# Kernel tuning notes

Hardware: AMD Instinct MI355X
Metric: run time of the kernel (lower is better)

The kernel has to match this reference:

```python
import jax, jax.numpy as jnp
import numpy as np

B, N, DIM, H = 8, 2048, 64, 8  # per-head dim == DIM (module convention: inner_dim = dim * n_heads)


def setup_inputs() -> dict:
    key = jax.random.key(0)
    k1, k2, k3 = jax.random.split(key, 3)
    x = jax.random.normal(k1, (B, N, DIM), dtype=jnp.float32)
    W_qkv = jax.random.normal(k2, (DIM, 3 * H * DIM), dtype=jnp.float32) * (DIM ** -0.5)
    W_out = jax.random.normal(k3, (H * DIM, DIM), dtype=jnp.float32) * ((H * DIM) ** -0.5)
    b_out = jnp.zeros((DIM,), dtype=jnp.float32)
    return {"x": x, "W_qkv": W_qkv, "W_out": W_out, "b_out": b_out}


def reference(x, W_qkv, W_out, b_out):
    b, n, d = x.shape
    h = W_qkv.shape[1] // (3 * d)
    qkv = x @ W_qkv                                   # [b, n, 3*h*d]
    q, k, v = jnp.split(qkv, 3, axis=-1)              # each [b, n, h*d]
    def to_heads(t):
        return t.reshape(b, n, h, d).transpose(0, 2, 1, 3)  # [b, h, n, d]
    q, k, v = map(to_heads, (q, k, v))
    scale = d ** -0.5
    dot = jnp.einsum('bhid,bhjd->bhij', q, k) * scale  # [b, h, n, n]
    A = jax.nn.softmax(dot, axis=-1)
    z = jnp.einsum('bhij,bhjd->bhid', A, v)            # [b, h, n, d]
    z = z.transpose(0, 2, 1, 3).reshape(b, n, h * d)   # [b, n, h*d]
    return z @ W_out + b_out                           # [b, n, d]
```

## Files before the change

### kernel.cpp

```cpp
#include <hip/hip_runtime.h>
#include <math.h>

#define BB 8
#define NN 2048
#define DD 64
#define HH 8
#define BH (BB*HH)
#define HD (HH*DD)
#define NROWS (BB*NN)
#define QKV_COLS (3*HD)

typedef __bf16 bf16_8 __attribute__((ext_vector_type(8)));
typedef __bf16 bf16_4 __attribute__((ext_vector_type(4)));
typedef float  f32_16 __attribute__((ext_vector_type(16)));
typedef float  f32_4  __attribute__((ext_vector_type(4)));

__device__ __forceinline__ unsigned pack_bf16(float a, float b) {
  union { __bf16 h[2]; unsigned u; } t;
  t.h[0] = (__bf16)a; t.h[1] = (__bf16)b;
  return t.u;
}

__global__ __launch_bounds__(256) void wtrans_kernel(
    const float* __restrict__ Wqkv, const float* __restrict__ Wout,
    __bf16* __restrict__ Wtq, __bf16* __restrict__ Wto) {
  int idx = blockIdx.x * 256 + threadIdx.x;
  if (idx < 64 * QKV_COLS) {
    int k = idx / QKV_COLS, col = idx % QKV_COLS;
    float v = Wqkv[idx];
    if (col < HD) v *= 0.125f;
    Wtq[col * 64 + k] = (__bf16)v;
  } else {
    int j = idx - 64 * QKV_COLS;
    int k = j >> 6, col = j & 63;
    Wto[col * 512 + k] = (__bf16)Wout[j];
  }
}

__global__ __launch_bounds__(256) void qkv_kernel(
    const float* __restrict__ x, const __bf16* __restrict__ Wtq,
    __bf16* __restrict__ Q, __bf16* __restrict__ K, __bf16* __restrict__ V) {
  const int lane = threadIdx.x & 63;
  const int wave = threadIdx.x >> 6;
  const int l31  = lane & 31, lhi = lane >> 5;
  const int cg   = blockIdx.x;
  const int row0 = blockIdx.y * 128 + wave * 32;

  const float* xr = x + (size_t)(row0 + l31) * 64 + lhi * 8;
  bf16_8 af[4];
#pragma unroll
  for (int s = 0; s < 4; s++) {
    f32_4 a0 = *(const f32_4*)(xr + s * 16);
    f32_4 a1 = *(const f32_4*)(xr + s * 16 + 4);
#pragma unroll
    for (int j = 0; j < 4; j++) { af[s][j] = (__bf16)a0[j]; af[s][4 + j] = (__bf16)a1[j]; }
  }

  f32_16 C0, C1;
#pragma unroll
  for (int i = 0; i < 16; i++) { C0[i] = 0.f; C1[i] = 0.f; }

  const __bf16* wb = Wtq + (size_t)cg * 64 * 64 + lhi * 8;
#pragma unroll
  for (int s = 0; s < 4; s++) {
    bf16_8 b0 = *(const bf16_8*)(wb + (size_t)l31 * 64 + s * 16);
    bf16_8 b1 = *(const bf16_8*)(wb + (size_t)(32 + l31) * 64 + s * 16);
    C0 = __builtin_amdgcn_mfma_f32_32x32x16_bf16(af[s], b0, C0, 0, 0, 0);
    C1 = __builtin_amdgcn_mfma_f32_32x32x16_bf16(af[s], b1, C1, 0, 0, 0);
  }

  const int col0  = cg * 64;
  const int which = col0 >> 9;
  const int h     = (col0 >> 6) & 7;
  __bf16* dst = (which == 0) ? Q : ((which == 1) ? K : V);
#pragma unroll
  for (int r = 0; r < 16; r++) {
    int n  = row0 + (r & 3) + 8 * (r >> 2) + 4 * lhi;
    int b  = n >> 11;
    int nn = n & 2047;
    size_t base = (((size_t)(b * HH + h) * NN) + nn) * DD;
    dst[base + l31]      = (__bf16)C0[r];
    dst[base + 32 + l31] = (__bf16)C1[r];
  }
}

__global__ __launch_bounds__(256) void vtrans_kernel(
    const __bf16* __restrict__ V, __bf16* __restrict__ Vt) {
  __shared__ __bf16 T[64 * 72];
  const int bh = blockIdx.x >> 5;
  const int n0 = (blockIdx.x & 31) * 64;
  const __bf16* src = V  + (size_t)bh * NN * DD;
  __bf16*       dst = Vt + (size_t)bh * DD * NN;

#pragma unroll
  for (int i = 0; i < 2; i++) {
    int c = threadIdx.x + i * 256;
    int r = c >> 3, c8 = (c & 7) * 8;
    *(bf16_8*)(&T[r * 72 + c8]) = *(const bf16_8*)(src + (size_t)(n0 + r) * DD + c8);
  }
  __syncthreads();
#pragma unroll
  for (int i = 0; i < 2; i++) {
    int c = threadIdx.x + i * 256;
    int d = c >> 3, j8 = (c & 7) * 8;
    bf16_8 o;
#pragma unroll
    for (int j = 0; j < 8; j++) o[j] = T[(j8 + j) * 72 + d];
    *(bf16_8*)(dst + (size_t)d * NN + n0 + j8) = o;
  }
}

__global__ __launch_bounds__(256, 4) void attn_kernel(
    const __bf16* __restrict__ Q, const __bf16* __restrict__ K,
    const __bf16* __restrict__ Vt, __bf16* __restrict__ z) {
  __shared__ __bf16 Ks[64 * 72];
  __shared__ __bf16 Vs[64 * 72];

  const int tid  = threadIdx.x;
  const int wave = tid >> 6;
  const int lane = tid & 63;
  const int l31  = lane & 31;
  const int lhi  = lane >> 5;
  const int xl   = lane ^ 32;
  const int bh   = blockIdx.x >> 4;
  const int q0   = (blockIdx.x & 15) * 128 + wave * 32;

  const __bf16* Qbase = Q + ((size_t)bh * NN + q0 + l31) * DD + lhi * 8;
  bf16_8 qf[4];
#pragma unroll
  for (int s = 0; s < 4; s++) qf[s] = *(const bf16_8*)(Qbase + s * 16);

  f32_16 O0, O1;
#pragma unroll
  for (int i = 0; i < 16; i++) { O0[i] = 0.f; O1[i] = 0.f; }
  float lsum = 0.f;

  const __bf16* Kb = K  + (size_t)bh * NN * DD;
  const __bf16* Vb = Vt + (size_t)bh * DD * NN;

  for (int kt = 0; kt < NN; kt += 64) {
    __syncthreads();
#pragma unroll
    for (int i = 0; i < 2; i++) {
      int c = tid + i * 256;
      int r = c >> 3, c8 = (c & 7) * 8;
      *(bf16_8*)(&Ks[r * 72 + c8]) = *(const bf16_8*)(Kb + (size_t)(kt + r) * DD + c8);
      *(bf16_8*)(&Vs[r * 72 + c8]) = *(const bf16_8*)(Vb + (size_t)r * NN + kt + c8);
    }
    __syncthreads();

    f32_16 S0, S1;
#pragma unroll
    for (int i = 0; i < 16; i++) { S0[i] = 0.f; S1[i] = 0.f; }
#pragma unroll
    for (int s = 0; s < 4; s++) {
      bf16_8 kb0 = *(const bf16_8*)(&Ks[l31 * 72 + s * 16 + lhi * 8]);
      bf16_8 kb1 = *(const bf16_8*)(&Ks[(32 + l31) * 72 + s * 16 + lhi * 8]);
      S0 = __builtin_amdgcn_mfma_f32_32x32x16_bf16(kb0, qf[s], S0, 0, 0, 0);
      S1 = __builtin_amdgcn_mfma_f32_32x32x16_bf16(kb1, qf[s], S1, 0, 0, 0);
    }

    unsigned pk[16];
#pragma unroll
    for (int t = 0; t < 8; t++) {
      float a = __expf(S0[2 * t]), b = __expf(S0[2 * t + 1]);
      float c = __expf(S1[2 * t]), d = __expf(S1[2 * t + 1]);
      lsum += (a + b) + (c + d);
      pk[t]     = pack_bf16(a, b);
      pk[8 + t] = pack_bf16(c, d);
    }

#pragma unroll
    for (int half = 0; half < 2; half++) {
#pragma unroll
      for (int st = 0; st < 2; st++) {
        const int base = half * 8 + st * 4;
        unsigned a0 = pk[base + 0], a1 = pk[base + 1];
        unsigned a2 = pk[base + 2], a3 = pk[base + 3];
        unsigned w0 = (unsigned)__shfl((int)a0, xl, 64);
        unsigned w1 = (unsigned)__shfl((int)a1, xl, 64);
        unsigned w2 = (unsigned)__shfl((int)a2, xl, 64);
        unsigned w3 = (unsigned)__shfl((int)a3, xl, 64);
        union { unsigned u[4]; bf16_8 v; } F;
        F.u[0] = lhi ? w2 : a0;
        F.u[1] = lhi ? w3 : a1;
        F.u[2] = lhi ? a2 : w0;
        F.u[3] = lhi ? a3 : w1;
        const int ks = half * 2 + st;
        bf16_8 va0 = *(const bf16_8*)(&Vs[l31 * 72 + ks * 16 + lhi * 8]);
        bf16_8 va1 = *(const bf16_8*)(&Vs[(32 + l31) * 72 + ks * 16 + lhi * 8]);
        O0 = __builtin_amdgcn_mfma_f32_32x32x16_bf16(va0, F.v, O0, 0, 0, 0);
        O1 = __builtin_amdgcn_mfma_f32_32x32x16_bf16(va1, F.v, O1, 0, 0, 0);
      }
    }
  }

  lsum += __shfl_xor(lsum, 32, 64);
  const float inv = 1.f / lsum;

  __syncthreads();
  __bf16* ow = ((wave & 2) ? Vs : Ks) + (wave & 1) * (32 * 72);
#pragma unroll
  for (int g = 0; g < 4; g++) {
    bf16_4 p0, p1;
#pragma unroll
    for (int i = 0; i < 4; i++) {
      p0[i] = (__bf16)(O0[4 * g + i] * inv);
      p1[i] = (__bf16)(O1[4 * g + i] * inv);
    }
    const int d0 = 8 * g + 4 * lhi;
    *(bf16_4*)(ow + l31 * 72 + d0)      = p0;
    *(bf16_4*)(ow + l31 * 72 + 32 + d0) = p1;
  }
  __syncthreads();

  const int b = bh >> 3, h = bh & 7;
  const int qr = lane >> 1, c0 = (lane & 1) * 32;
  __bf16* zp = z + ((size_t)b * NN + q0 + qr) * HD + h * DD + c0;
#pragma unroll
  for (int j = 0; j < 4; j++) {
    *(bf16_8*)(zp + 8 * j) = *(const bf16_8*)(ow + qr * 72 + c0 + 8 * j);
  }
}

__global__ __launch_bounds__(64) void out_proj_kernel(
    const __bf16* __restrict__ z, const __bf16* __restrict__ Wto,
    const float* __restrict__ bout, float* __restrict__ out) {
  const int lane = threadIdx.x;
  const int l31  = lane & 31, lhi = lane >> 5;
  const int row0 = blockIdx.x * 32;

  const __bf16* zr = z   + (size_t)(row0 + l31) * HD + lhi * 8;
  const __bf16* w0 = Wto + (size_t)l31 * HD + lhi * 8;
  const __bf16* w1 = Wto + (size_t)(32 + l31) * HD + lhi * 8;

  f32_16 C0, C1;
#pragma unroll
  for (int i = 0; i < 16; i++) { C0[i] = 0.f; C1[i] = 0.f; }

#pragma unroll
  for (int s = 0; s < 32; s++) {
    bf16_8 a  = *(const bf16_8*)(zr + s * 16);
    bf16_8 b0 = *(const bf16_8*)(w0 + s * 16);
    bf16_8 b1 = *(const bf16_8*)(w1 + s * 16);
    C0 = __builtin_amdgcn_mfma_f32_32x32x16_bf16(a, b0, C0, 0, 0, 0);
    C1 = __builtin_amdgcn_mfma_f32_32x32x16_bf16(a, b1, C1, 0, 0, 0);
  }

  const float bi0 = bout[l31];
  const float bi1 = bout[32 + l31];
#pragma unroll
  for (int r = 0; r < 16; r++) {
    int n = row0 + (r & 3) + 8 * (r >> 2) + 4 * lhi;
    out[(size_t)n * 64 + l31]      = C0[r] + bi0;
    out[(size_t)n * 64 + 32 + l31] = C1[r] + bi1;
  }
}

extern "C" void kernel_launch(void* const* d_in, const int* in_sizes, int n_in,
                              void* d_out, int out_size, void* d_ws, size_t ws_size,
                              hipStream_t stream) {
  const float* x    = (const float*)d_in[0];
  const float* Wqkv = (const float*)d_in[1];
  const float* Wout = (const float*)d_in[2];
  const float* bout = (const float*)d_in[3];
  float* out = (float*)d_out;

  const size_t buf_elems = (size_t)BB * HH * NN * DD;
  __bf16* Qw  = (__bf16*)d_ws;
  __bf16* Kw  = Qw  + buf_elems;
  __bf16* Vw  = Kw  + buf_elems;
  __bf16* Vtw = Vw  + buf_elems;
  __bf16* zw  = Vtw + buf_elems;
  __bf16* Wtq = zw  + buf_elems;
  __bf16* Wto = Wtq + (size_t)QKV_COLS * 64;

  wtrans_kernel<<<512, 256, 0, stream>>>(Wqkv, Wout, Wtq, Wto);
  qkv_kernel<<<dim3(QKV_COLS / 64, NROWS / 128), 256, 0, stream>>>(x, Wtq, Qw, Kw, Vw);
  vtrans_kernel<<<BH * (NN / 64), 256, 0, stream>>>(Vw, Vtw);
  attn_kernel<<<BH * (NN / 128), 256, 0, stream>>>(Qw, Kw, Vtw, zw);
  out_proj_kernel<<<NROWS / 32, 64, 0, stream>>>(zw, Wto, bout, out);
}
```

Baseline: 206.5 us.

## Fuse V transpose into QKV, prefetch 128-key tiles, use exp2 and permlane swap

```diff
diff --git a/kernel.cpp b/kernel.cpp
--- a/kernel.cpp
+++ b/kernel.cpp
@@ -14,11 +14,20 @@
 typedef __bf16 bf16_4 __attribute__((ext_vector_type(4)));
 typedef float  f32_16 __attribute__((ext_vector_type(16)));
 typedef float  f32_4  __attribute__((ext_vector_type(4)));
+typedef int    i32_2  __attribute__((ext_vector_type(2)));
 
 __device__ __forceinline__ unsigned pack_bf16(float a, float b) {
   union { __bf16 h[2]; unsigned u; } t;
   t.h[0] = (__bf16)a; t.h[1] = (__bf16)b;
   return t.u;
+}
+
+__device__ __forceinline__ float fast_exp2(float x) {
+#if __has_builtin(__builtin_amdgcn_exp2f)
+  return __builtin_amdgcn_exp2f(x);
+#else
+  return __expf(x * 0.69314718056f);
+#endif
 }
 
 __global__ __launch_bounds__(256) void wtrans_kernel(
@@ -28,8 +37,9 @@
   if (idx < 64 * QKV_COLS) {
     int k = idx / QKV_COLS, col = idx % QKV_COLS;
     float v = Wqkv[idx];
-    if (col < HD) v *= 0.125f;
+    if (col < HD) v *= 0.125f * 1.44269504088896f;
     Wtq[col * 64 + k] = (__bf16)v;
+    (void)k;
   } else {
     int j = idx - 64 * QKV_COLS;
     int k = j >> 6, col = j & 63;
@@ -39,7 +49,8 @@
 
 __global__ __launch_bounds__(256) void qkv_kernel(
     const float* __restrict__ x, const __bf16* __restrict__ Wtq,
-    __bf16* __restrict__ Q, __bf16* __restrict__ K, __bf16* __restrict__ V) {
+    __bf16* __restrict__ Q, __bf16* __restrict__ K, __bf16* __restrict__ Vt) {
+  __shared__ __bf16 T[4][64][34];
   const int lane = threadIdx.x & 63;
   const int wave = threadIdx.x >> 6;
   const int l31  = lane & 31, lhi = lane >> 5;
@@ -72,49 +83,39 @@
   const int col0  = cg * 64;
   const int which = col0 >> 9;
   const int h     = (col0 >> 6) & 7;
-  __bf16* dst = (which == 0) ? Q : ((which == 1) ? K : V);
-#pragma unroll
-  for (int r = 0; r < 16; r++) {
-    int n  = row0 + (r & 3) + 8 * (r >> 2) + 4 * lhi;
-    int b  = n >> 11;
-    int nn = n & 2047;
-    size_t base = (((size_t)(b * HH + h) * NN) + nn) * DD;
-    dst[base + l31]      = (__bf16)C0[r];
-    dst[base + 32 + l31] = (__bf16)C1[r];
-  }
-}
-
-__global__ __launch_bounds__(256) void vtrans_kernel(
-    const __bf16* __restrict__ V, __bf16* __restrict__ Vt) {
-  __shared__ __bf16 T[64 * 72];
-  const int bh = blockIdx.x >> 5;
-  const int n0 = (blockIdx.x & 31) * 64;
-  const __bf16* src = V  + (size_t)bh * NN * DD;
-  __bf16*       dst = Vt + (size_t)bh * DD * NN;
-
-#pragma unroll
-  for (int i = 0; i < 2; i++) {
-    int c = threadIdx.x + i * 256;
-    int r = c >> 3, c8 = (c & 7) * 8;
-    *(bf16_8*)(&T[r * 72 + c8]) = *(const bf16_8*)(src + (size_t)(n0 + r) * DD + c8);
-  }
-  __syncthreads();
-#pragma unroll
-  for (int i = 0; i < 2; i++) {
-    int c = threadIdx.x + i * 256;
-    int d = c >> 3, j8 = (c & 7) * 8;
-    bf16_8 o;
-#pragma unroll
-    for (int j = 0; j < 8; j++) o[j] = T[(j8 + j) * 72 + d];
-    *(bf16_8*)(dst + (size_t)d * NN + n0 + j8) = o;
-  }
-}
-
-__global__ __launch_bounds__(256, 4) void attn_kernel(
+  const int b     = row0 >> 11;
+  const int n0l   = row0 & 2047;
+
+  if (which < 2) {
+    __bf16* dst = (which == 0) ? Q : K;
+#pragma unroll
+    for (int r = 0; r < 16; r++) {
+      int nl = (r & 3) + 8 * (r >> 2) + 4 * lhi;
+      size_t base = (((size_t)(b * HH + h) * NN) + n0l + nl) * DD;
+      dst[base + l31]      = (__bf16)C0[r];
+      dst[base + 32 + l31] = (__bf16)C1[r];
+    }
+  } else {
+    __bf16 (*Tw)[34] = T[wave];
+#pragma unroll
+    for (int r = 0; r < 16; r++) {
+      int nl = (r & 3) + 8 * (r >> 2) + 4 * lhi;
+      Tw[l31][nl]      = (__bf16)C0[r];
+      Tw[32 + l31][nl] = (__bf16)C1[r];
+    }
+    __bf16* dst = Vt + (((size_t)(b * HH + h) * DD) + lane) * NN + n0l;
+#pragma unroll
+    for (int j = 0; j < 4; j++) {
+      *(bf16_8*)(dst + j * 8) = *(const bf16_8*)(&Tw[lane][j * 8]);
+    }
+  }
+}
+
+__global__ __launch_bounds__(256, 3) void attn_kernel(
     const __bf16* __restrict__ Q, const __bf16* __restrict__ K,
     const __bf16* __restrict__ Vt, __bf16* __restrict__ z) {
-  __shared__ __bf16 Ks[64 * 72];
-  __shared__ __bf16 Vs[64 * 72];
+  __shared__ __bf16 Ks[128 * 72];
+  __shared__ __bf16 Vs[64 * 136];
 
   const int tid  = threadIdx.x;
   const int wave = tid >> 6;
@@ -133,73 +134,100 @@
   f32_16 O0, O1;
 #pragma unroll
   for (int i = 0; i < 16; i++) { O0[i] = 0.f; O1[i] = 0.f; }
-  float lsum = 0.f;
+  float ls0 = 0.f, ls1 = 0.f;
 
   const __bf16* Kb = K  + (size_t)bh * NN * DD;
   const __bf16* Vb = Vt + (size_t)bh * DD * NN;
 
-  for (int kt = 0; kt < NN; kt += 64) {
+  const int krow = tid >> 3, kcol = (tid & 7) * 8;
+  const int vrow = tid >> 4, vcol = (tid & 15) * 8;
+  const __bf16* kgl = Kb + krow * 64 + kcol;
+  const __bf16* vgl = Vb + (size_t)vrow * NN + vcol;
+  __bf16* klds = &Ks[krow * 72 + kcol];
+  __bf16* vlds = &Vs[vrow * 136 + vcol];
+
+  bf16_8 gk[4], gv[4];
+#pragma unroll
+  for (int i = 0; i < 4; i++) {
+    gk[i] = *(const bf16_8*)(kgl + i * 32 * 64);
+    gv[i] = *(const bf16_8*)(vgl + i * 16 * NN);
+  }
+
+  for (int kt = 0; kt < NN; kt += 128) {
     __syncthreads();
 #pragma unroll
-    for (int i = 0; i < 2; i++) {
-      int c = tid + i * 256;
-      int r = c >> 3, c8 = (c & 7) * 8;
-      *(bf16_8*)(&Ks[r * 72 + c8]) = *(const bf16_8*)(Kb + (size_t)(kt + r) * DD + c8);
-      *(bf16_8*)(&Vs[r * 72 + c8]) = *(const bf16_8*)(Vb + (size_t)r * NN + kt + c8);
+    for (int i = 0; i < 4; i++) {
+      *(bf16_8*)(klds + i * 32 * 72)  = gk[i];
+      *(bf16_8*)(vlds + i * 16 * 136) = gv[i];
     }
     __syncthreads();
-
-    f32_16 S0, S1;
-#pragma unroll
-    for (int i = 0; i < 16; i++) { S0[i] = 0.f; S1[i] = 0.f; }
-#pragma unroll
-    for (int s = 0; s < 4; s++) {
-      bf16_8 kb0 = *(const bf16_8*)(&Ks[l31 * 72 + s * 16 + lhi * 8]);
-      bf16_8 kb1 = *(const bf16_8*)(&Ks[(32 + l31) * 72 + s * 16 + lhi * 8]);
-      S0 = __builtin_amdgcn_mfma_f32_32x32x16_bf16(kb0, qf[s], S0, 0, 0, 0);
-      S1 = __builtin_amdgcn_mfma_f32_32x32x16_bf16(kb1, qf[s], S1, 0, 0, 0);
-    }
-
-    unsigned pk[16];
-#pragma unroll
-    for (int t = 0; t < 8; t++) {
-      float a = __expf(S0[2 * t]), b = __expf(S0[2 * t + 1]);
-      float c = __expf(S1[2 * t]), d = __expf(S1[2 * t + 1]);
-      lsum += (a + b) + (c + d);
-      pk[t]     = pack_bf16(a, b);
-      pk[8 + t] = pack_bf16(c, d);
-    }
-
-#pragma unroll
-    for (int half = 0; half < 2; half++) {
-#pragma unroll
-      for (int st = 0; st < 2; st++) {
-        const int base = half * 8 + st * 4;
-        unsigned a0 = pk[base + 0], a1 = pk[base + 1];
-        unsigned a2 = pk[base + 2], a3 = pk[base + 3];
-        unsigned w0 = (unsigned)__shfl((int)a0, xl, 64);
-        unsigned w1 = (unsigned)__shfl((int)a1, xl, 64);
-        unsigned w2 = (unsigned)__shfl((int)a2, xl, 64);
-        unsigned w3 = (unsigned)__shfl((int)a3, xl, 64);
+    if (kt + 128 < NN) {
+#pragma unroll
+      for (int i = 0; i < 4; i++) {
+        gk[i] = *(const bf16_8*)(kgl + (kt + 128) * 64 + i * 32 * 64);
+        gv[i] = *(const bf16_8*)(vgl + (kt + 128) + i * 16 * NN);
+      }
+    }
+
+#pragma unroll
+    for (int hf = 0; hf < 2; hf++) {
+      f32_16 S0, S1;
+#pragma unroll
+      for (int i = 0; i < 16; i++) { S0[i] = 0.f; S1[i] = 0.f; }
+#pragma unroll
+      for (int s = 0; s < 4; s++) {
+        bf16_8 kb0 = *(const bf16_8*)(&Ks[(hf * 64 + l31) * 72 + s * 16 + lhi * 8]);
+        bf16_8 kb1 = *(const bf16_8*)(&Ks[(hf * 64 + 32 + l31) * 72 + s * 16 + lhi * 8]);
+        S0 = __builtin_amdgcn_mfma_f32_32x32x16_bf16(kb0, qf[s], S0, 0, 0, 0);
+        S1 = __builtin_amdgcn_mfma_f32_32x32x16_bf16(kb1, qf[s], S1, 0, 0, 0);
+      }
+
+      unsigned pk[16];
+#pragma unroll
+      for (int t = 0; t < 8; t++) {
+        float a = fast_exp2(S0[2 * t]), b = fast_exp2(S0[2 * t + 1]);
+        float c = fast_exp2(S1[2 * t]), d = fast_exp2(S1[2 * t + 1]);
+        ls0 += a + b;
+        ls1 += c + d;
+        pk[t]     = pack_bf16(a, b);
+        pk[8 + t] = pack_bf16(c, d);
+      }
+
+#pragma unroll
+      for (int g = 0; g < 4; g++) {
+        const int base = (g >> 1) * 8 + (g & 1) * 4;
+        int a0 = (int)pk[base + 0], a1 = (int)pk[base + 1];
+        int a2 = (int)pk[base + 2], a3 = (int)pk[base + 3];
         union { unsigned u[4]; bf16_8 v; } F;
-        F.u[0] = lhi ? w2 : a0;
-        F.u[1] = lhi ? w3 : a1;
-        F.u[2] = lhi ? a2 : w0;
-        F.u[3] = lhi ? a3 : w1;
-        const int ks = half * 2 + st;
-        bf16_8 va0 = *(const bf16_8*)(&Vs[l31 * 72 + ks * 16 + lhi * 8]);
-        bf16_8 va1 = *(const bf16_8*)(&Vs[(32 + l31) * 72 + ks * 16 + lhi * 8]);
+#if __has_builtin(__builtin_amdgcn_permlane32_swap)
+        i32_2 r02 = __builtin_amdgcn_permlane32_swap(a0, a2, false, false);
+        i32_2 r13 = __builtin_amdgcn_permlane32_swap(a1, a3, false, false);
+        F.u[0] = (unsigned)r02.x; F.u[2] = (unsigned)r02.y;
+        F.u[1] = (unsigned)r13.x; F.u[3] = (unsigned)r13.y;
+#else
+        unsigned w0 = (unsigned)__shfl(a0, xl, 64);
+        unsigned w1 = (unsigned)__shfl(a1, xl, 64);
+        unsigned w2 = (unsigned)__shfl(a2, xl, 64);
+        unsigned w3 = (unsigned)__shfl(a3, xl, 64);
+        F.u[0] = lhi ? w2 : (unsigned)a0;
+        F.u[1] = lhi ? w3 : (unsigned)a1;
+        F.u[2] = lhi ? (unsigned)a2 : w0;
+        F.u[3] = lhi ? (unsigned)a3 : w1;
+#endif
+        bf16_8 va0 = *(const bf16_8*)(&Vs[l31 * 136 + hf * 64 + g * 16 + lhi * 8]);
+        bf16_8 va1 = *(const bf16_8*)(&Vs[(32 + l31) * 136 + hf * 64 + g * 16 + lhi * 8]);
         O0 = __builtin_amdgcn_mfma_f32_32x32x16_bf16(va0, F.v, O0, 0, 0, 0);
         O1 = __builtin_amdgcn_mfma_f32_32x32x16_bf16(va1, F.v, O1, 0, 0, 0);
       }
     }
   }
 
+  float lsum = ls0 + ls1;
   lsum += __shfl_xor(lsum, 32, 64);
   const float inv = 1.f / lsum;
 
   __syncthreads();
-  __bf16* ow = ((wave & 2) ? Vs : Ks) + (wave & 1) * (32 * 72);
+  __bf16* ow = Ks + wave * (32 * 72);
 #pragma unroll
   for (int g = 0; g < 4; g++) {
     bf16_4 p0, p1;
@@ -212,8 +240,6 @@
     *(bf16_4*)(ow + l31 * 72 + d0)      = p0;
     *(bf16_4*)(ow + l31 * 72 + 32 + d0) = p1;
   }
-  __syncthreads();
-
   const int b = bh >> 3, h = bh & 7;
   const int qr = lane >> 1, c0 = (lane & 1) * 32;
   __bf16* zp = z + ((size_t)b * NN + q0 + qr) * HD + h * DD + c0;
@@ -223,23 +249,26 @@
   }
 }
 
-__global__ __launch_bounds__(64) void out_proj_kernel(
+__global__ __launch_bounds__(256) void out_proj_kernel(
     const __bf16* __restrict__ z, const __bf16* __restrict__ Wto,
     const float* __restrict__ bout, float* __restrict__ out) {
-  const int lane = threadIdx.x;
+  __shared__ float red[2][64][36];
+  const int tid  = threadIdx.x;
+  const int wave = tid >> 6, lane = tid & 63;
+  const int rt   = wave >> 1, kh = wave & 1;
   const int l31  = lane & 31, lhi = lane >> 5;
-  const int row0 = blockIdx.x * 32;
-
-  const __bf16* zr = z   + (size_t)(row0 + l31) * HD + lhi * 8;
-  const __bf16* w0 = Wto + (size_t)l31 * HD + lhi * 8;
-  const __bf16* w1 = Wto + (size_t)(32 + l31) * HD + lhi * 8;
+  const int row0 = blockIdx.x * 64 + rt * 32;
+
+  const __bf16* zr = z   + (size_t)(row0 + l31) * HD + kh * 256 + lhi * 8;
+  const __bf16* w0 = Wto + (size_t)l31 * HD        + kh * 256 + lhi * 8;
+  const __bf16* w1 = Wto + (size_t)(32 + l31) * HD + kh * 256 + lhi * 8;
 
   f32_16 C0, C1;
 #pragma unroll
   for (int i = 0; i < 16; i++) { C0[i] = 0.f; C1[i] = 0.f; }
 
 #pragma unroll
-  for (int s = 0; s < 32; s++) {
+  for (int s = 0; s < 16; s++) {
     bf16_8 a  = *(const bf16_8*)(zr + s * 16);
     bf16_8 b0 = *(const bf16_8*)(w0 + s * 16);
     bf16_8 b1 = *(const bf16_8*)(w1 + s * 16);
@@ -247,13 +276,20 @@
     C1 = __builtin_amdgcn_mfma_f32_32x32x16_bf16(a, b1, C1, 0, 0, 0);
   }
 
-  const float bi0 = bout[l31];
-  const float bi1 = bout[32 + l31];
-#pragma unroll
-  for (int r = 0; r < 16; r++) {
-    int n = row0 + (r & 3) + 8 * (r >> 2) + 4 * lhi;
-    out[(size_t)n * 64 + l31]      = C0[r] + bi0;
-    out[(size_t)n * 64 + 32 + l31] = C1[r] + bi1;
+  float* rw = &red[rt][lane][0];
+  if (kh) {
+#pragma unroll
+    for (int r = 0; r < 16; r++) { rw[r] = C0[r]; rw[16 + r] = C1[r]; }
+  }
+  __syncthreads();
+  if (!kh) {
+    const float bi0 = bout[l31], bi1 = bout[32 + l31];
+#pragma unroll
+    for (int r = 0; r < 16; r++) {
+      int n = row0 + (r & 3) + 8 * (r >> 2) + 4 * lhi;
+      out[(size_t)n * 64 + l31]      = C0[r] + rw[r]      + bi0;
+      out[(size_t)n * 64 + 32 + l31] = C1[r] + rw[16 + r] + bi1;
+    }
   }
 }
 
@@ -269,15 +305,13 @@
   const size_t buf_elems = (size_t)BB * HH * NN * DD;
   __bf16* Qw  = (__bf16*)d_ws;
   __bf16* Kw  = Qw  + buf_elems;
-  __bf16* Vw  = Kw  + buf_elems;
-  __bf16* Vtw = Vw  + buf_elems;
+  __bf16* Vtw = Kw  + buf_elems;
   __bf16* zw  = Vtw + buf_elems;
   __bf16* Wtq = zw  + buf_elems;
   __bf16* Wto = Wtq + (size_t)QKV_COLS * 64;
 
   wtrans_kernel<<<512, 256, 0, stream>>>(Wqkv, Wout, Wtq, Wto);
-  qkv_kernel<<<dim3(QKV_COLS / 64, NROWS / 128), 256, 0, stream>>>(x, Wtq, Qw, Kw, Vw);
-  vtrans_kernel<<<BH * (NN / 64), 256, 0, stream>>>(Vw, Vtw);
+  qkv_kernel<<<dim3(QKV_COLS / 64, NROWS / 128), 256, 0, stream>>>(x, Wtq, Qw, Kw, Vtw);
   attn_kernel<<<BH * (NN / 128), 256, 0, stream>>>(Qw, Kw, Vtw, zw);
-  out_proj_kernel<<<NROWS / 32, 64, 0, stream>>>(zw, Wto, bout, out);
-}
+  out_proj_kernel<<<NROWS / 64, 256, 0, stream>>>(zw, Wto, bout, out);
+}
```

Result: faster. 192.9 us (-6.6%).
